# Kernel optimization log

Hardware: AMD Instinct MI355X
Metric: run time of the kernel (lower is better)

Reference implementation:

```python
import jax, jax.numpy as jnp
import numpy as np

TOPK = 32

def softsign(x):
    return x / (1.0 + jnp.abs(x))

def setup_inputs() -> dict:
    key = jax.random.key(0)
    k1, k2, k3 = jax.random.split(key, 3)
    B, Q, S, D = 1, 4096, 32768, 256
    return {
        "query_val": jax.random.normal(k1, (B, Q, D), dtype=jnp.float32),
        "source_val": jax.random.normal(k2, (B, S, D), dtype=jnp.float32),
        "source_state": jax.random.normal(k3, (B, S), dtype=jnp.float32),
    }

def reference(query_val, source_val, source_state):
    # pairwise scores (dot-product similarity): [B, Q, S]
    scores = jnp.einsum("bqd,bsd->bqs", query_val, source_val)
    # global top-k over sources == streaming blockwise top-k merge in the original
    top_scores, top_idx = jax.lax.top_k(scores, TOPK)  # [B, Q, K]
    edges = softsign(top_scores)                        # edge_compress_fn
    # gather_state_by_indices: [B, Q, K]
    sel_state = jnp.take_along_axis(source_state[:, None, :], top_idx, axis=-1)
    # gather_val_by_indices: [B, Q, K, D]
    sel_val = jnp.take_along_axis(source_val[:, None, :, :], top_idx[..., None], axis=2)
    delta_state = jnp.sum(edges * sel_state, axis=-1)          # [B, Q]
    delta_val = jnp.sum(edges[..., None] * sel_val, axis=-2)   # [B, Q, D]
    return delta_state, delta_val
```

## Files before the change

### kernel.cpp

```cpp
#include <hip/hip_runtime.h>
#include <stdint.h>

typedef unsigned int u32;
typedef unsigned long long u64;
typedef unsigned short u16;
typedef unsigned char u8;

#define NQ 4096
#define NS 32768
#define ND 256
#define TOPK 32
#define CAP 256
#define CAP2 24
#define ZT 2.75f

#define QB 256
#define SB 32
#define NSLICE 32
#define SLICE (NS / NSLICE)
#define CH (SLICE / SB)

typedef __attribute__((ext_vector_type(8))) __bf16 bf16x8;
typedef __attribute__((ext_vector_type(4))) float f32x4;

#define QB_OFF   (NS * ND * 2)
#define TQ_OFF   (QB_OFF + NQ * ND * 2)
#define C8_OFF   (TQ_OFF + NQ * 4)
#define CD_OFF   (C8_OFF + NQ * NSLICE)

__device__ __forceinline__ u16 f2bf(float x) {
  u32 u = __float_as_uint(x);
  u32 r = u + 0x7FFFu + ((u >> 16) & 1u);
  return (u16)(r >> 16);
}

__global__ void k_prep_src(const float* __restrict__ src, uint4* __restrict__ dst) {
  int t = blockIdx.x * 256 + threadIdx.x;
  const float4* s4 = (const float4*)src + (size_t)t * 2;
  float4 a = s4[0], b = s4[1];
  uint4 o;
  o.x = (u32)f2bf(a.x) | ((u32)f2bf(a.y) << 16);
  o.y = (u32)f2bf(a.z) | ((u32)f2bf(a.w) << 16);
  o.z = (u32)f2bf(b.x) | ((u32)f2bf(b.y) << 16);
  o.w = (u32)f2bf(b.z) | ((u32)f2bf(b.w) << 16);
  dst[t] = o;
}

__global__ void k_prep_q(const float* __restrict__ qv, u16* __restrict__ qb,
                         float* __restrict__ tq) {
  int lane = threadIdx.x & 63, w = threadIdx.x >> 6;
  int q = blockIdx.x * 4 + w;
  float4 v = *((const float4*)(qv + (size_t)q * ND) + lane);
  uint2 p;
  p.x = (u32)f2bf(v.x) | ((u32)f2bf(v.y) << 16);
  p.y = (u32)f2bf(v.z) | ((u32)f2bf(v.w) << 16);
  *((uint2*)(qb + (size_t)q * ND) + lane) = p;
  float s = v.x * v.x + v.y * v.y + v.z * v.z + v.w * v.w;
  #pragma unroll
  for (int o = 1; o < 64; o <<= 1) s += __shfl_xor(s, o, 64);
  if (lane == 0) tq[q] = ZT * sqrtf(s);
}

__global__ __launch_bounds__(256, 2) void k_screen(
    const u16* __restrict__ qb, const u16* __restrict__ srcb,
    const float* __restrict__ tq, u8* __restrict__ cnt8, u32* __restrict__ cand2) {
  __shared__ __align__(16) u16 lds[2][SB * ND];
  __shared__ u32 bcnt[QB];
  const int tid  = threadIdx.x;
  const int lane = tid & 63;
  const int w    = tid >> 6;
  const int l15  = lane & 15, lhi = lane >> 4;

  const int id   = blockIdx.x;
  const int xcd  = id & 7;
  const int rank = id >> 3;
  const int by   = xcd * 4 + (rank >> 4);
  const int bx   = rank & 15;

  const int qbase = bx * QB + w * 64;
  const int sbase = by * SLICE;

  bcnt[tid] = 0u;

  bf16x8 afrag[4][8];
  float  thr[4][4];
  #pragma unroll
  for (int mt = 0; mt < 4; ++mt) {
    const u16* qp = qb + (size_t)(qbase + mt * 16 + l15) * ND;
    #pragma unroll
    for (int ks = 0; ks < 8; ++ks)
      afrag[mt][ks] = *((const bf16x8*)(qp + ks * 32 + lhi * 8));
    #pragma unroll
    for (int r = 0; r < 4; ++r) thr[mt][r] = tq[qbase + mt * 16 + lhi * 4 + r];
  }

  int goff[4];
  #pragma unroll
  for (int i = 0; i < 4; ++i) {
    int slot = i * 256 + tid;
    int row  = slot >> 5;
    int o    = (slot & 31) ^ (row & 7);
    goff[i]  = row * ND + o * 8;
  }

#define STAGE(b, c)                                                              \
  {                                                                              \
    const u16* sp_ = srcb + (size_t)(sbase + (c) * SB) * ND;                     \
    _Pragma("unroll")                                                            \
    for (int i_ = 0; i_ < 4; ++i_)                                               \
      __builtin_amdgcn_global_load_lds(                                          \
          (const __attribute__((address_space(1))) void*)(sp_ + goff[i_]),       \
          (__attribute__((address_space(3))) void*)(&lds[b][(i_ * 256 + tid) * 8]), \
          16, 0, 0);                                                             \
  }

#define COMPUTE(b, srow0)                                                        \
  {                                                                              \
    f32x4 acc[4][2];                                                             \
    _Pragma("unroll")                                                            \
    for (int mt = 0; mt < 4; ++mt)                                               \
      _Pragma("unroll")                                                          \
      for (int nt = 0; nt < 2; ++nt) acc[mt][nt] = (f32x4){0.f, 0.f, 0.f, 0.f};  \
    _Pragma("unroll")                                                            \
    for (int ks = 0; ks < 8; ++ks) {                                             \
      bf16x8 bfr[2];                                                             \
      _Pragma("unroll")                                                          \
      for (int nt = 0; nt < 2; ++nt) {                                           \
        int r_ = nt * 16 + l15;                                                  \
        int o_ = ks * 4 + lhi;                                                   \
        int slot_ = r_ * 32 + (o_ ^ (r_ & 7));                                   \
        bfr[nt] = *((const bf16x8*)(&lds[b][slot_ * 8]));                        \
      }                                                                          \
      _Pragma("unroll")                                                          \
      for (int mt = 0; mt < 4; ++mt)                                             \
        _Pragma("unroll")                                                        \
        for (int nt = 0; nt < 2; ++nt)                                           \
          acc[mt][nt] = __builtin_amdgcn_mfma_f32_16x16x32_bf16(                 \
              afrag[mt][ks], bfr[nt], acc[mt][nt], 0, 0, 0);                     \
    }                                                                            \
    _Pragma("unroll")                                                            \
    for (int mt = 0; mt < 4; ++mt)                                               \
      _Pragma("unroll")                                                          \
      for (int nt = 0; nt < 2; ++nt)                                             \
        _Pragma("unroll")                                                        \
        for (int r_ = 0; r_ < 4; ++r_) {                                         \
          float sc_ = acc[mt][nt][r_];                                           \
          if (sc_ > thr[mt][r_]) {                                               \
            int ql_ = w * 64 + mt * 16 + lhi * 4 + r_;                           \
            u32 off_ = atomicAdd(&bcnt[ql_], 1u);                                \
            if (off_ < CAP2)                                                     \
              cand2[(((size_t)(qbase + mt * 16 + lhi * 4 + r_)) * NSLICE + by) * CAP2 + off_] = \
                  ((u32)((srow0) + nt * 16 + l15) << 16) | (u32)f2bf(sc_);       \
          }                                                                      \
        }                                                                        \
  }

  STAGE(0, 0);
  __syncthreads();
  int cur = 0;
  for (int c = 0; c < CH - 1; ++c) {
    STAGE(cur ^ 1, c + 1);
    COMPUTE(cur, sbase + c * SB);
    __syncthreads();
    cur ^= 1;
  }
  COMPUTE(cur, sbase + (CH - 1) * SB);
#undef STAGE
#undef COMPUTE

  __syncthreads();
  {
    u32 c = bcnt[tid];
    cnt8[(size_t)by * NQ + bx * QB + tid] = (u8)(c < CAP2 ? c : CAP2);
  }
}

__global__ __launch_bounds__(256) void k_finish(
    const float* __restrict__ qval, const float* __restrict__ sval,
    const float* __restrict__ sstate, const u8* __restrict__ cnt8,
    const u32* __restrict__ cand2, float* __restrict__ out) {
  const int q = blockIdx.x;
  const int tid = threadIdx.x;
  const int lane = tid & 63, w = tid >> 6;
  __shared__ u16  scnt[NSLICE];
  __shared__ u16  soff[NSLICE];
  __shared__ u32  skey[CAP];
  __shared__ u32  sidxl[CAP];
  __shared__ float sexact[64];
  __shared__ u32  ssrc[64];
  __shared__ float fw[TOPK];
  __shared__ u32  fi[TOPK];

  if (tid < NSLICE) scnt[tid] = cnt8[(size_t)tid * NQ + q];
  skey[tid] = 0u;
  __syncthreads();
  if (tid == 0) {
    u32 a = 0;
    #pragma unroll
    for (int s = 0; s < NSLICE; ++s) { soff[s] = (u16)a; a += scnt[s]; }
  }
  __syncthreads();

  {
    int s = tid >> 3, j0 = tid & 7;
    #pragma unroll
    for (int rep = 0; rep < 3; ++rep) {
      int j = j0 + rep * 8;
      if (j < (int)scnt[s]) {
        int p = (int)soff[s] + j;
        if (p < CAP) {
          u32 ent = cand2[((size_t)q * NSLICE + s) * CAP2 + j];
          skey[p]  = ((ent & 0xFFFFu) << 8) | (u32)p;
          sidxl[p] = ent >> 16;
        }
      }
    }
  }
  __syncthreads();

  for (int k = 2; k <= 256; k <<= 1) {
    for (int j = k >> 1; j > 0; j >>= 1) {
      int p = tid ^ j;
      u32 a = skey[tid], b = skey[p];
      bool keepMax = ((tid < p) == ((tid & k) == 0));
      u32 r = keepMax ? (a > b ? a : b) : (a > b ? b : a);
      __syncthreads();
      skey[tid] = r;
      __syncthreads();
    }
  }

  const int l16 = lane & 15, sub = lane >> 4;
  float4 qf[4];
  #pragma unroll
  for (int j = 0; j < 4; ++j)
    qf[j] = *((const float4*)(qval + (size_t)q * ND) + l16 * 4 + j);
  #pragma unroll
  for (int p = 0; p < 4; ++p) {
    int e = w * 16 + p * 4 + sub;
    u32 key = skey[e];
    u32 si = sidxl[key & 0xFFu];
    float dp = 0.f;
    if (key) {
      const float4* vp = (const float4*)(sval + (size_t)si * ND) + l16 * 4;
      #pragma unroll
      for (int j = 0; j < 4; ++j) {
        float4 v = vp[j];
        dp += qf[j].x * v.x + qf[j].y * v.y + qf[j].z * v.z + qf[j].w * v.w;
      }
    }
    #pragma unroll
    for (int o = 1; o < 16; o <<= 1) dp += __shfl_xor(dp, o, 64);
    if (l16 == 0) { sexact[e] = key ? dp : -3.0e38f; ssrc[e] = si; }
  }
  __syncthreads();

  if (w == 0) {
    float sc = sexact[lane];
    u32 si  = ssrc[lane];
    u32 kb  = __float_as_uint(sc);
    kb = kb ^ (u32)(((int)kb >> 31) | 0x80000000);
    u64 kk = ((u64)kb << 32) | (u32)(~si);
    #pragma unroll
    for (int k = 2; k <= 64; k <<= 1) {
      #pragma unroll
      for (int j = k >> 1; j > 0; j >>= 1) {
        u64 o = __shfl_xor(kk, j, 64);
        bool keepMax = (((lane & j) == 0) == ((lane & k) == 0));
        kk = keepMax ? (kk > o ? kk : o) : (kk > o ? o : kk);
      }
    }
    u32 si2 = ~((u32)kk);
    u32 kb2 = (u32)(kk >> 32);
    u32 fb  = (kb2 & 0x80000000u) ? (kb2 ^ 0x80000000u) : ~kb2;
    float s = __uint_as_float(fb);
    bool ok = (lane < TOPK) && (s > -1.0e38f);
    float edge = ok ? (s / (1.f + fabsf(s))) : 0.f;
    float contrib = ok ? edge * sstate[si2] : 0.f;
    if (lane < TOPK) { fw[lane] = edge; fi[lane] = ok ? si2 : 0u; }
    #pragma unroll
    for (int o = 1; o < 64; o <<= 1) contrib += __shfl_xor(contrib, o, 64);
    if (lane == 0) out[q] = contrib;
  }
  __syncthreads();

  float acc = 0.f;
  #pragma unroll 8
  for (int k = 0; k < TOPK; ++k)
    acc += fw[k] * sval[(size_t)fi[k] * ND + tid];
  out[NQ + (size_t)q * ND + tid] = acc;
}

extern "C" void kernel_launch(void* const* d_in, const int* in_sizes, int n_in,
                              void* d_out, int out_size, void* d_ws, size_t ws_size,
                              hipStream_t stream) {
  const float* qval   = (const float*)d_in[0];
  const float* sval   = (const float*)d_in[1];
  const float* sstate = (const float*)d_in[2];
  float* out = (float*)d_out;
  char*  ws  = (char*)d_ws;
  u16*   srcb  = (u16*)ws;
  u16*   qbuf  = (u16*)(ws + QB_OFF);
  float* tq    = (float*)(ws + TQ_OFF);
  u8*    cnt8  = (u8*)(ws + C8_OFF);
  u32*   cand2 = (u32*)(ws + CD_OFF);

  k_prep_src<<<(NS * ND / 8) / 256, 256, 0, stream>>>(sval, (uint4*)srcb);
  k_prep_q<<<NQ / 4, 256, 0, stream>>>(qval, qbuf, tq);
  k_screen<<<(NQ / QB) * NSLICE, 256, 0, stream>>>(qbuf, srcb, tq, cnt8, cand2);
  k_finish<<<NQ, 256, 0, stream>>>(qval, sval, sstate, cnt8, cand2, out);
}
```

Measured before the change: 153.2 us.

## Give each wave private LDS double-buffer and drop block-wide syncs in screen loop

The screening kernel stops sharing one block-wide double buffer of 32 source rows. Each wave now streams its own 16-row tiles into a private double buffer using global_load_lds, with explicit vmcnt waits in place of __syncthreads. Removing block barriers lets waves run independently and overlap loads with MFMA. In exchange, each wave loads the same source rows separately, which quadruples global and L2 traffic for the source tile. The hand-written waitcnt counts must also stay correct for this to work.

```diff
diff --git a/kernel.cpp b/kernel.cpp
--- a/kernel.cpp
+++ b/kernel.cpp
@@ -15,10 +15,10 @@
 #define ZT 2.75f
 
 #define QB 256
-#define SB 32
 #define NSLICE 32
 #define SLICE (NS / NSLICE)
-#define CH (SLICE / SB)
+#define SB2 16
+#define CH2 (SLICE / SB2)
 
 typedef __attribute__((ext_vector_type(8))) __bf16 bf16x8;
 typedef __attribute__((ext_vector_type(4))) float f32x4;
@@ -64,7 +64,7 @@
 __global__ __launch_bounds__(256, 2) void k_screen(
     const u16* __restrict__ qb, const u16* __restrict__ srcb,
     const float* __restrict__ tq, u8* __restrict__ cnt8, u32* __restrict__ cand2) {
-  __shared__ __align__(16) u16 lds[2][SB * ND];
+  __shared__ __align__(16) u16 lds[4][2][SB2 * ND];
   __shared__ u32 bcnt[QB];
   const int tid  = threadIdx.x;
   const int lane = tid & 63;
@@ -94,79 +94,75 @@
     for (int r = 0; r < 4; ++r) thr[mt][r] = tq[qbase + mt * 16 + lhi * 4 + r];
   }
 
-  int goff[4];
-  #pragma unroll
-  for (int i = 0; i < 4; ++i) {
-    int slot = i * 256 + tid;
+  int goff[8];
+  #pragma unroll
+  for (int i = 0; i < 8; ++i) {
+    int slot = i * 64 + lane;
     int row  = slot >> 5;
     int o    = (slot & 31) ^ (row & 7);
     goff[i]  = row * ND + o * 8;
   }
 
-#define STAGE(b, c)                                                              \
+#define STAGEW(BUF, c)                                                           \
   {                                                                              \
-    const u16* sp_ = srcb + (size_t)(sbase + (c) * SB) * ND;                     \
-    _Pragma("unroll")                                                            \
-    for (int i_ = 0; i_ < 4; ++i_)                                               \
+    const u16* sp_ = srcb + (size_t)(sbase + (c) * SB2) * ND;                    \
+    _Pragma("unroll")                                                            \
+    for (int i_ = 0; i_ < 8; ++i_)                                               \
       __builtin_amdgcn_global_load_lds(                                          \
           (const __attribute__((address_space(1))) void*)(sp_ + goff[i_]),       \
-          (__attribute__((address_space(3))) void*)(&lds[b][(i_ * 256 + tid) * 8]), \
+          (__attribute__((address_space(3))) void*)(&lds[w][BUF][i_ * 512]),     \
           16, 0, 0);                                                             \
   }
 
-#define COMPUTE(b, srow0)                                                        \
+#define ITER(c, BUF, VN, DOSTAGE)                                                \
   {                                                                              \
-    f32x4 acc[4][2];                                                             \
+    asm volatile("s_waitcnt vmcnt(" VN ")" ::: "memory");                        \
+    __builtin_amdgcn_sched_barrier(0);                                           \
+    const int srow0 = sbase + (c) * SB2;                                         \
+    bf16x8 bfr[8];                                                               \
+    _Pragma("unroll")                                                            \
+    for (int ks = 0; ks < 8; ++ks) {                                             \
+      int o_ = ks * 4 + lhi;                                                     \
+      int slot_ = l15 * 32 + (o_ ^ (l15 & 7));                                   \
+      bfr[ks] = *((const bf16x8*)(&lds[w][BUF][slot_ * 8]));                     \
+    }                                                                            \
+    f32x4 acc[4];                                                                \
+    _Pragma("unroll")                                                            \
+    for (int mt = 0; mt < 4; ++mt) acc[mt] = (f32x4){0.f, 0.f, 0.f, 0.f};        \
+    _Pragma("unroll")                                                            \
+    for (int ks = 0; ks < 8; ++ks)                                               \
+      _Pragma("unroll")                                                          \
+      for (int mt = 0; mt < 4; ++mt)                                             \
+        acc[mt] = __builtin_amdgcn_mfma_f32_16x16x32_bf16(                       \
+            afrag[mt][ks], bfr[ks], acc[mt], 0, 0, 0);                           \
+    asm volatile("s_waitcnt lgkmcnt(0)" ::: "memory");                           \
+    __builtin_amdgcn_sched_barrier(0);                                           \
+    if (DOSTAGE) STAGEW(BUF, (c) + 2);                                           \
     _Pragma("unroll")                                                            \
     for (int mt = 0; mt < 4; ++mt)                                               \
       _Pragma("unroll")                                                          \
-      for (int nt = 0; nt < 2; ++nt) acc[mt][nt] = (f32x4){0.f, 0.f, 0.f, 0.f};  \
-    _Pragma("unroll")                                                            \
-    for (int ks = 0; ks < 8; ++ks) {                                             \
-      bf16x8 bfr[2];                                                             \
-      _Pragma("unroll")                                                          \
-      for (int nt = 0; nt < 2; ++nt) {                                           \
-        int r_ = nt * 16 + l15;                                                  \
-        int o_ = ks * 4 + lhi;                                                   \
-        int slot_ = r_ * 32 + (o_ ^ (r_ & 7));                                   \
-        bfr[nt] = *((const bf16x8*)(&lds[b][slot_ * 8]));                        \
+      for (int r_ = 0; r_ < 4; ++r_) {                                           \
+        float sc_ = acc[mt][r_];                                                 \
+        if (sc_ > thr[mt][r_]) {                                                 \
+          int ql_ = w * 64 + mt * 16 + lhi * 4 + r_;                             \
+          u32 off_ = atomicAdd(&bcnt[ql_], 1u);                                  \
+          if (off_ < CAP2)                                                       \
+            cand2[(((size_t)(qbase + mt * 16 + lhi * 4 + r_)) * NSLICE + by) * CAP2 + off_] = \
+                ((u32)(srow0 + l15) << 16) | (u32)f2bf(sc_);                     \
+        }                                                                        \
       }                                                                          \
-      _Pragma("unroll")                                                          \
-      for (int mt = 0; mt < 4; ++mt)                                             \
-        _Pragma("unroll")                                                        \
-        for (int nt = 0; nt < 2; ++nt)                                           \
-          acc[mt][nt] = __builtin_amdgcn_mfma_f32_16x16x32_bf16(                 \
-              afrag[mt][ks], bfr[nt], acc[mt][nt], 0, 0, 0);                     \
-    }                                                                            \
-    _Pragma("unroll")                                                            \
-    for (int mt = 0; mt < 4; ++mt)                                               \
-      _Pragma("unroll")                                                          \
-      for (int nt = 0; nt < 2; ++nt)                                             \
-        _Pragma("unroll")                                                        \
-        for (int r_ = 0; r_ < 4; ++r_) {                                         \
-          float sc_ = acc[mt][nt][r_];                                           \
-          if (sc_ > thr[mt][r_]) {                                               \
-            int ql_ = w * 64 + mt * 16 + lhi * 4 + r_;                           \
-            u32 off_ = atomicAdd(&bcnt[ql_], 1u);                                \
-            if (off_ < CAP2)                                                     \
-              cand2[(((size_t)(qbase + mt * 16 + lhi * 4 + r_)) * NSLICE + by) * CAP2 + off_] = \
-                  ((u32)((srow0) + nt * 16 + l15) << 16) | (u32)f2bf(sc_);       \
-          }                                                                      \
-        }                                                                        \
-  }
-
-  STAGE(0, 0);
-  __syncthreads();
-  int cur = 0;
-  for (int c = 0; c < CH - 1; ++c) {
-    STAGE(cur ^ 1, c + 1);
-    COMPUTE(cur, sbase + c * SB);
-    __syncthreads();
-    cur ^= 1;
-  }
-  COMPUTE(cur, sbase + (CH - 1) * SB);
-#undef STAGE
-#undef COMPUTE
+  }
+
+  STAGEW(0, 0);
+  STAGEW(1, 1);
+  for (int cc = 0; cc < 31; ++cc) {
+    ITER(2 * cc,     0, "8", 1);
+    ITER(2 * cc + 1, 1, "8", 1);
+  }
+  ITER(62, 0, "8", 0);
+  ITER(63, 1, "0", 0);
+#undef STAGEW
+#undef ITER
 
   __syncthreads();
   {
```

Result: slower. 165.4 us (+8.0%).
